# Kernel tuning notes

Measured on AMD Instinct MI355X. Metric: run time of the kernel, lower is better.

## Reference

```python
import jax, jax.numpy as jnp
import numpy as np

U = 100001          # user_count = user_num + 1
I = 50001           # item_count = item_num + 1
N = U + I           # total nodes
D = 64              # embedding dim
E = 3_200_000       # user-item interactions
NNZ = 2 * E         # symmetric directed edges
N_LAYERS = 3


def setup_inputs() -> dict:
    key = jax.random.key(0)
    k1, k2, k3, k4 = jax.random.split(key, 4)
    user_emb = jax.random.normal(k1, (U, D), dtype=jnp.float32) * 0.1
    item_emb = jax.random.normal(k2, (I, D), dtype=jnp.float32) * 0.1
    # random bipartite interactions, symmetrized like _get_a_adj_matrix
    u = jax.random.randint(k3, (E,), 0, U, dtype=jnp.int32)
    it = jax.random.randint(k4, (E,), 0, I, dtype=jnp.int32)
    rows = jnp.concatenate([u, it + U])            # [NNZ]
    cols = jnp.concatenate([it + U, u])            # [NNZ]
    # D^{-1/2} A D^{-1/2}: deg from row sums of A (values are 1s, duplicates sum)
    deg = jax.ops.segment_sum(jnp.ones((NNZ,), jnp.float32), rows, num_segments=N) + 1e-7
    dinv = deg ** -0.5
    vals = dinv[rows] * dinv[cols]                 # [NNZ]
    return {"user_emb": user_emb, "item_emb": item_emb,
            "rows": rows, "cols": cols, "vals": vals}


def _spmm(rows, cols, vals, x):
    # out[r] += vals * x[c]  (COO SpMM via gather + segment_sum)
    return jax.ops.segment_sum(vals[:, None] * x[cols], rows, num_segments=N)


def reference(user_emb, item_emb, rows, cols, vals):
    all_emb = jnp.concatenate([user_emb, item_emb], axis=0)   # [N, D]
    acc = all_emb                                             # running sum over layers (== mean * (L+1))
    h = all_emb
    for _ in range(N_LAYERS):
        h = _spmm(rows, cols, vals, h)
        acc = acc + h
    out = acc / (N_LAYERS + 1)                                # mean over stacked layers
    return out[:U], out[U:]
```

## Files before the change

### kernel.cpp

```cpp
#include <hip/hip_runtime.h>
#include <hip/hip_fp16.h>

#define U_CNT 100001
#define I_CNT 50001
#define N_CNT 150002
#define DIM 64
#define BROWS 128
#define NB2 ((N_CNT + BROWS - 1) / BROWS)
#define NB2R 1176
#define CH 6144
#define OUTCAP 10240

__device__ inline __half2 u2h(unsigned int u) { union { unsigned int u; __half2 h; } c; c.u = u; return c.h; }
__device__ inline unsigned int h2u(__half2 h) { union { unsigned int u; __half2 h; } c; c.h = h; return c.u; }

typedef float f4_t __attribute__((ext_vector_type(4)));
typedef unsigned int u4_t __attribute__((ext_vector_type(4)));

__device__ inline float4 ntload_f4(const float4* p) {
    f4_t v = __builtin_nontemporal_load((const f4_t*)p);
    return make_float4(v.x, v.y, v.z, v.w);
}
__device__ inline void ntstore_f4(float4* p, float4 v) {
    f4_t t; t.x = v.x; t.y = v.y; t.z = v.z; t.w = v.w;
    __builtin_nontemporal_store(t, (f4_t*)p);
}
__device__ inline void ntstore_u4(uint4* p, uint4 v) {
    u4_t t; t.x = v.x; t.y = v.y; t.z = v.z; t.w = v.w;
    __builtin_nontemporal_store(t, (u4_t*)p);
}

__global__ void bucket_hist(const int* __restrict__ rows, int* __restrict__ bhist,
                            int nnz) {
    __shared__ int lh[NB2];
    for (int i = threadIdx.x; i < NB2; i += blockDim.x) lh[i] = 0;
    __syncthreads();
    int stride = gridDim.x * blockDim.x;
    for (int i = blockIdx.x * blockDim.x + threadIdx.x; i < nnz; i += stride)
        atomicAdd(&lh[rows[i] >> 7], 1);
    __syncthreads();
    for (int i = threadIdx.x; i < NB2; i += blockDim.x) {
        int v = lh[i];
        if (v) atomicAdd(&bhist[i], v);
    }
}

__global__ void bucket_scan(const int* __restrict__ bhist,
                            int* __restrict__ bucket_ptr,
                            int* __restrict__ bcur) {
    __shared__ int aux[256];
    int t = threadIdx.x;
    int v[8];
    int s = 0;
    int b8 = t * 8;
    if (t < 147) {
        #pragma unroll
        for (int k = 0; k < 8; ++k) {
            int i = b8 + k;
            int d = (i < NB2) ? bhist[i] : 0;
            v[k] = s;
            s += d;
        }
    }
    aux[t] = s;
    __syncthreads();
    for (int off = 1; off < 256; off <<= 1) {
        int x = (t >= off) ? aux[t - off] : 0;
        __syncthreads();
        aux[t] += x;
        __syncthreads();
    }
    if (t < 147) {
        int gb = (t > 0) ? aux[t - 1] : 0;
        #pragma unroll
        for (int k = 0; k < 8; ++k) {
            int i = b8 + k;
            if (i < NB2) {
                int ex = gb + v[k];
                bucket_ptr[i] = ex;
                bcur[i] = ex;
            }
        }
    }
    if (t == 255) bucket_ptr[NB2] = aux[255];
}

__global__ void __launch_bounds__(256) partition_kernel(
    const int* __restrict__ rows, const int* __restrict__ cols,
    int* __restrict__ bcur, unsigned int* __restrict__ staging, int nnz)
{
    __shared__ int hist[NB2R];
    __shared__ int aux[256];
    __shared__ int gbase[NB2];
    __shared__ unsigned int recs[CH];
    __shared__ unsigned short guess[CH / 8];
    const int t = threadIdx.x;
    int base = blockIdx.x * CH;
    int lim = nnz - base; if (lim > CH) lim = CH;

    for (int i = t; i < NB2R; i += 256) hist[i] = 0;
    __syncthreads();
    for (int i = t; i < lim; i += 256)
        atomicAdd(&hist[rows[base + i] >> 7], 1);
    __syncthreads();
    {
        int s = 0;
        if (t < 147) {
            int b8 = t * 8;
            #pragma unroll
            for (int k = 0; k < 8; ++k) s += hist[b8 + k];
        }
        aux[t] = s;
    }
    __syncthreads();
    for (int off = 1; off < 256; off <<= 1) {
        int x = (t >= off) ? aux[t - off] : 0;
        __syncthreads();
        aux[t] += x;
        __syncthreads();
    }
    if (t < 147) {
        int run = (t > 0) ? aux[t - 1] : 0;
        int b8 = t * 8;
        #pragma unroll
        for (int k = 0; k < 8; ++k) {
            run += hist[b8 + k];
            hist[b8 + k] = run;
        }
    }
    __syncthreads();
    for (int i = t; i < NB2; i += 256) {
        int hi_ = hist[i];
        int lo_ = (i > 0) ? hist[i - 1] : 0;
        for (int m = (lo_ + 7) & ~7; m < hi_; m += 8)
            guess[m >> 3] = (unsigned short)i;
        int cnt = hi_ - lo_;
        if (cnt) gbase[i] = atomicAdd(&bcur[i], cnt);
    }
    __syncthreads();
    for (int i = t; i < lim; i += 256) {
        int r = rows[base + i];
        int c = cols[base + i];
        int p = atomicAdd(&hist[r >> 7], -1) - 1;
        recs[p] = ((unsigned int)c << 7) | (unsigned int)(r & (BROWS - 1));
    }
    __syncthreads();
    for (int p = t; p < lim; p += 256) {
        unsigned int rec = recs[p];
        int lo = guess[p >> 3];
        while (hist[lo + 1] <= p) ++lo;
        staging[gbase[lo] + (p - hist[lo])] = rec;
    }
}

__global__ void __launch_bounds__(256) binplace_kernel(
    const int* __restrict__ bucket_ptr,
    const unsigned int* __restrict__ staging,
    unsigned int* __restrict__ col_s,
    int* __restrict__ row_ptr,
    float* __restrict__ dinv) {
    __shared__ int hist[BROWS];
    __shared__ int cur[BROWS];
    __shared__ unsigned int outb[OUTCAP];
    int b = blockIdx.x;
    int base = b << 7;
    int beg = bucket_ptr[b];
    int end = bucket_ptr[b + 1];
    int total = end - beg;
    int t = threadIdx.x;
    if (t < BROWS) hist[t] = 0;
    __syncthreads();
    for (int j = beg + t; j < end; j += 256)
        atomicAdd(&hist[staging[j] & (BROWS - 1u)], 1);
    __syncthreads();
    int cnt = (t < BROWS) ? hist[t] : 0;
    for (int off = 1; off < BROWS; off <<= 1) {
        int v = (t < BROWS && t >= off) ? hist[t - off] : 0;
        __syncthreads();
        if (t < BROWS) hist[t] += v;
        __syncthreads();
    }
    if (t < BROWS) {
        int startl = hist[t] - cnt;
        cur[t] = startl;
        int r = base + t;
        if (r < N_CNT) {
            row_ptr[r] = beg + startl;
            dinv[r] = 1.0f / sqrtf((float)cnt + 1e-7f);
        }
    }
    if (b == NB2 - 1 && t == 0) row_ptr[N_CNT] = end;
    __syncthreads();
    if (total <= OUTCAP) {
        for (int j = beg + t; j < end; j += 256) {
            unsigned int rec = staging[j];
            int pos = atomicAdd(&cur[rec & (BROWS - 1u)], 1);
            outb[pos] = rec >> 7;
        }
        __syncthreads();
        for (int k = t; k < total; k += 256)
            col_s[beg + k] = outb[k];
    } else {
        for (int j = beg + t; j < end; j += 256) {
            unsigned int rec = staging[j];
            int pos = atomicAdd(&cur[rec & (BROWS - 1u)], 1);
            col_s[beg + pos] = rec >> 7;
        }
    }
}

__global__ void init_kernel(const float4* __restrict__ ue,
                            const float4* __restrict__ ie,
                            const float* __restrict__ dinv,
                            uint4* __restrict__ hs) {
    int i = blockIdx.x * blockDim.x + threadIdx.x;
    if (i >= N_CNT * 8) return;
    int node = i >> 3;
    int s = i & 7;
    float d = dinv[node];
    size_t fo = (size_t)node * 16 + s * 2;
    float4 v0, v1;
    if (node < U_CNT) { v0 = ntload_f4(&ue[fo]); v1 = ntload_f4(&ue[fo + 1]); }
    else { size_t io = fo - (size_t)U_CNT * 16; v0 = ntload_f4(&ie[io]); v1 = ntload_f4(&ie[io + 1]); }
    uint4 h;
    h.x = h2u(__floats2half2_rn(d * v0.x, d * v0.y));
    h.y = h2u(__floats2half2_rn(d * v0.z, d * v0.w));
    h.z = h2u(__floats2half2_rn(d * v1.x, d * v1.y));
    h.w = h2u(__floats2half2_rn(d * v1.z, d * v1.w));
    hs[(size_t)node * 8 + s] = h;
}

__device__ inline void acc8(float4& a0, float4& a1, uint4 u) {
    float2 f;
    f = __half22float2(u2h(u.x)); a0.x += f.x; a0.y += f.y;
    f = __half22float2(u2h(u.y)); a0.z += f.x; a0.w += f.y;
    f = __half22float2(u2h(u.z)); a1.x += f.x; a1.y += f.y;
    f = __half22float2(u2h(u.w)); a1.z += f.x; a1.w += f.y;
}

__global__ void spmm_gather(const int* __restrict__ row_ptr,
                            const unsigned int* __restrict__ col_s,
                            const float* __restrict__ dinv,
                            const uint4* __restrict__ x,
                            uint4* __restrict__ y,
                            const uint4* __restrict__ h1s,
                            const float4* __restrict__ ue,
                            const float4* __restrict__ ie,
                            float4* __restrict__ acc,
                            int r0, int r1, int last) {
    int r = r0 + blockIdx.x * 32 + (threadIdx.x >> 3);
    int s = threadIdx.x & 7;
    if (r >= r1) return;
    int beg = row_ptr[r];
    int end = row_ptr[r + 1];
    float4 a0 = {0.f, 0.f, 0.f, 0.f}, a1 = {0.f, 0.f, 0.f, 0.f};
    float4 b0 = {0.f, 0.f, 0.f, 0.f}, b1 = {0.f, 0.f, 0.f, 0.f};
    int j = beg;
    for (; j + 8 <= end; j += 8) {
        unsigned int c0 = col_s[j];
        unsigned int c1 = col_s[j + 1];
        unsigned int c2 = col_s[j + 2];
        unsigned int c3 = col_s[j + 3];
        unsigned int c4 = col_s[j + 4];
        unsigned int c5 = col_s[j + 5];
        unsigned int c6 = col_s[j + 6];
        unsigned int c7 = col_s[j + 7];
        uint4 u0 = x[(size_t)c0 * 8 + s];
        uint4 u1 = x[(size_t)c1 * 8 + s];
        uint4 u2 = x[(size_t)c2 * 8 + s];
        uint4 u3 = x[(size_t)c3 * 8 + s];
        uint4 u4 = x[(size_t)c4 * 8 + s];
        uint4 u5 = x[(size_t)c5 * 8 + s];
        uint4 u6 = x[(size_t)c6 * 8 + s];
        uint4 u7 = x[(size_t)c7 * 8 + s];
        acc8(a0, a1, u0);
        acc8(b0, b1, u1);
        acc8(a0, a1, u2);
        acc8(b0, b1, u3);
        acc8(a0, a1, u4);
        acc8(b0, b1, u5);
        acc8(a0, a1, u6);
        acc8(b0, b1, u7);
    }
    for (; j + 4 <= end; j += 4) {
        unsigned int c0 = col_s[j];
        unsigned int c1 = col_s[j + 1];
        unsigned int c2 = col_s[j + 2];
        unsigned int c3 = col_s[j + 3];
        uint4 u0 = x[(size_t)c0 * 8 + s];
        uint4 u1 = x[(size_t)c1 * 8 + s];
        uint4 u2 = x[(size_t)c2 * 8 + s];
        uint4 u3 = x[(size_t)c3 * 8 + s];
        acc8(a0, a1, u0);
        acc8(b0, b1, u1);
        acc8(a0, a1, u2);
        acc8(b0, b1, u3);
    }
    for (; j < end; ++j) {
        unsigned int c0 = col_s[j];
        uint4 u0 = x[(size_t)c0 * 8 + s];
        acc8(a0, a1, u0);
    }
    a0.x += b0.x; a0.y += b0.y; a0.z += b0.z; a0.w += b0.w;
    a1.x += b1.x; a1.y += b1.y; a1.z += b1.z; a1.w += b1.w;

    float d = dinv[r];
    if (!last) {
        float d2 = d * d;
        uint4 h;
        h.x = h2u(__floats2half2_rn(d2 * a0.x, d2 * a0.y));
        h.y = h2u(__floats2half2_rn(d2 * a0.z, d2 * a0.w));
        h.z = h2u(__floats2half2_rn(d2 * a1.x, d2 * a1.y));
        h.w = h2u(__floats2half2_rn(d2 * a1.z, d2 * a1.w));
        ntstore_u4(&y[(size_t)r * 8 + s], h);
        return;
    }

    float inv = 1.0f / d;
    uint4 u1 = h1s[(size_t)r * 8 + s];
    uint4 u2v = x[(size_t)r * 8 + s];
    float4 s0 = {0.f, 0.f, 0.f, 0.f}, s1 = {0.f, 0.f, 0.f, 0.f};
    acc8(s0, s1, u1);
    acc8(s0, s1, u2v);
    size_t fo = (size_t)r * 16 + s * 2;
    float4 e0a, e0b;
    if (r < U_CNT) { e0a = ntload_f4(&ue[fo]); e0b = ntload_f4(&ue[fo + 1]); }
    else { size_t io = fo - (size_t)U_CNT * 16; e0a = ntload_f4(&ie[io]); e0b = ntload_f4(&ie[io + 1]); }
    float4 o0, o1;
    o0.x = 0.25f * (e0a.x + inv * s0.x + d * a0.x);
    o0.y = 0.25f * (e0a.y + inv * s0.y + d * a0.y);
    o0.z = 0.25f * (e0a.z + inv * s0.z + d * a0.z);
    o0.w = 0.25f * (e0a.w + inv * s0.w + d * a0.w);
    o1.x = 0.25f * (e0b.x + inv * s1.x + d * a1.x);
    o1.y = 0.25f * (e0b.y + inv * s1.y + d * a1.y);
    o1.z = 0.25f * (e0b.z + inv * s1.z + d * a1.z);
    o1.w = 0.25f * (e0b.w + inv * s1.w + d * a1.w);
    ntstore_f4(&acc[fo], o0);
    ntstore_f4(&acc[fo + 1], o1);
}

extern "C" void kernel_launch(void* const* d_in, const int* in_sizes, int n_in,
                              void* d_out, int out_size, void* d_ws, size_t ws_size,
                              hipStream_t stream) {
    const float* ue   = (const float*)d_in[0];
    const float* ie   = (const float*)d_in[1];
    const int*   rows = (const int*)d_in[2];
    const int*   cols = (const int*)d_in[3];
    int nnz = in_sizes[2];

    float* acc = (float*)d_out;

    unsigned int* ws = (unsigned int*)d_ws;
    uint4* hs0 = (uint4*)ws;
    uint4* hs1 = hs0 + (size_t)N_CNT * 8;
    int*   row_ptr    = (int*)(hs1 + (size_t)N_CNT * 8);
    int*   bhist      = row_ptr + (N_CNT + 1);
    int*   bucket_ptr = bhist + NB2;
    int*   bcur       = bucket_ptr + (NB2 + 1);
    float* dinv       = (float*)(bcur + NB2);
    unsigned int* staging = (unsigned int*)(dinv + N_CNT);
    unsigned int* col_s   = staging + nnz;

    const int tpb = 256;

    hipMemsetAsync(bhist, 0, NB2 * sizeof(int), stream);
    bucket_hist<<<512, tpb, 0, stream>>>(rows, bhist, nnz);
    bucket_scan<<<1, 256, 0, stream>>>(bhist, bucket_ptr, bcur);
    partition_kernel<<<(nnz + CH - 1) / CH, tpb, 0, stream>>>(
        rows, cols, bcur, staging, nnz);
    binplace_kernel<<<NB2, tpb, 0, stream>>>(
        bucket_ptr, staging, col_s, row_ptr, dinv);

    init_kernel<<<(N_CNT * 8 + tpb - 1) / tpb, tpb, 0, stream>>>(
        (const float4*)ue, (const float4*)ie, dinv, hs0);

    uint4* cur_h = hs0;
    uint4* nxt_h = hs1;
    const int ublocks = (U_CNT + 31) / 32;
    const int iblocks = (N_CNT - U_CNT + 31) / 32;
    for (int l = 0; l < 3; ++l) {
        int last = (l == 2) ? 1 : 0;
        spmm_gather<<<ublocks, tpb, 0, stream>>>(
            row_ptr, col_s, dinv, cur_h, nxt_h, nxt_h,
            (const float4*)ue, (const float4*)ie, (float4*)acc, 0, U_CNT, last);
        spmm_gather<<<iblocks, tpb, 0, stream>>>(
            row_ptr, col_s, dinv, cur_h, nxt_h, nxt_h,
            (const float4*)ue, (const float4*)ie, (float4*)acc, U_CNT, N_CNT, last);
        uint4* tmp = cur_h; cur_h = nxt_h; nxt_h = tmp;
    }
}
```

Measured before the change: 565.8 us.

## Replace atomic bucket offsets with deterministic per-chunk count-scan partition

New measurement: 537.4 us. 5.0% less time.

```diff
diff --git a/kernel.cpp b/kernel.cpp
--- a/kernel.cpp
+++ b/kernel.cpp
@@ -30,24 +30,51 @@
     __builtin_nontemporal_store(t, (u4_t*)p);
 }
 
-__global__ void bucket_hist(const int* __restrict__ rows, int* __restrict__ bhist,
-                            int nnz) {
-    __shared__ int lh[NB2];
-    for (int i = threadIdx.x; i < NB2; i += blockDim.x) lh[i] = 0;
-    __syncthreads();
-    int stride = gridDim.x * blockDim.x;
-    for (int i = blockIdx.x * blockDim.x + threadIdx.x; i < nnz; i += stride)
-        atomicAdd(&lh[rows[i] >> 7], 1);
-    __syncthreads();
-    for (int i = threadIdx.x; i < NB2; i += blockDim.x) {
-        int v = lh[i];
-        if (v) atomicAdd(&bhist[i], v);
-    }
+
+__global__ void count_kernel(const int* __restrict__ rows, int* __restrict__ cnt,
+                             int nnz) {
+    __shared__ int lh[NB2R];
+    int t = threadIdx.x;
+    for (int i = t; i < NB2R; i += 256) lh[i] = 0;
+    __syncthreads();
+    int base = blockIdx.x * CH;
+    int lim = nnz - base; if (lim > CH) lim = CH;
+    for (int i = t; i < lim; i += 256)
+        atomicAdd(&lh[rows[base + i] >> 7], 1);
+    __syncthreads();
+    int* row = cnt + (size_t)blockIdx.x * NB2R;
+    for (int i = t; i < NB2R; i += 256) row[i] = lh[i];
+}
+
+__global__ void scan_chunks(const int* __restrict__ cnt, int* __restrict__ ex2,
+                            int* __restrict__ bhist, int nchunk) {
+    __shared__ int aux[256];
+    int b = blockIdx.x;
+    int t = threadIdx.x;
+    int G = (nchunk + 255) >> 8;
+    int c0 = t * G;
+    int c1 = c0 + G; if (c1 > nchunk) c1 = nchunk;
+    int s = 0;
+    for (int ch = c0; ch < c1; ++ch) s += cnt[(size_t)ch * NB2R + b];
+    aux[t] = s;
+    __syncthreads();
+    for (int off = 1; off < 256; off <<= 1) {
+        int x = (t >= off) ? aux[t - off] : 0;
+        __syncthreads();
+        aux[t] += x;
+        __syncthreads();
+    }
+    int run = (t > 0) ? aux[t - 1] : 0;
+    for (int ch = c0; ch < c1; ++ch) {
+        int v = cnt[(size_t)ch * NB2R + b];
+        ex2[(size_t)b * nchunk + ch] = run;
+        run += v;
+    }
+    if (t == 255) bhist[b] = aux[255];
 }
 
 __global__ void bucket_scan(const int* __restrict__ bhist,
-                            int* __restrict__ bucket_ptr,
-                            int* __restrict__ bcur) {
+                            int* __restrict__ bucket_ptr) {
     __shared__ int aux[256];
     int t = threadIdx.x;
     int v[8];
@@ -75,19 +102,17 @@
         #pragma unroll
         for (int k = 0; k < 8; ++k) {
             int i = b8 + k;
-            if (i < NB2) {
-                int ex = gb + v[k];
-                bucket_ptr[i] = ex;
-                bcur[i] = ex;
-            }
+            if (i < NB2) bucket_ptr[i] = gb + v[k];
         }
     }
     if (t == 255) bucket_ptr[NB2] = aux[255];
 }
 
-__global__ void __launch_bounds__(256) partition_kernel(
+__global__ void __launch_bounds__(256) fill_kernel(
     const int* __restrict__ rows, const int* __restrict__ cols,
-    int* __restrict__ bcur, unsigned int* __restrict__ staging, int nnz)
+    const int* __restrict__ cnt, const int* __restrict__ ex2,
+    const int* __restrict__ bucket_ptr,
+    unsigned int* __restrict__ staging, int nnz, int nchunk)
 {
     __shared__ int hist[NB2R];
     __shared__ int aux[256];
@@ -95,13 +120,14 @@
     __shared__ unsigned int recs[CH];
     __shared__ unsigned short guess[CH / 8];
     const int t = threadIdx.x;
-    int base = blockIdx.x * CH;
+    int chunk = blockIdx.x;
+    int base = chunk * CH;
     int lim = nnz - base; if (lim > CH) lim = CH;
 
-    for (int i = t; i < NB2R; i += 256) hist[i] = 0;
-    __syncthreads();
-    for (int i = t; i < lim; i += 256)
-        atomicAdd(&hist[rows[base + i] >> 7], 1);
+    const int* crow = cnt + (size_t)chunk * NB2R;
+    for (int i = t; i < NB2R; i += 256) hist[i] = crow[i];
+    for (int i = t; i < NB2; i += 256)
+        gbase[i] = bucket_ptr[i] + ex2[(size_t)i * nchunk + chunk];
     __syncthreads();
     {
         int s = 0;
@@ -134,8 +160,6 @@
         int lo_ = (i > 0) ? hist[i - 1] : 0;
         for (int m = (lo_ + 7) & ~7; m < hi_; m += 8)
             guess[m >> 3] = (unsigned short)i;
-        int cnt = hi_ - lo_;
-        if (cnt) gbase[i] = atomicAdd(&bcur[i], cnt);
     }
     __syncthreads();
     for (int i = t; i < lim; i += 256) {
@@ -347,6 +371,7 @@
     const int*   rows = (const int*)d_in[2];
     const int*   cols = (const int*)d_in[3];
     int nnz = in_sizes[2];
+    int nchunk = (nnz + CH - 1) / CH;
 
     float* acc = (float*)d_out;
 
@@ -356,18 +381,19 @@
     int*   row_ptr    = (int*)(hs1 + (size_t)N_CNT * 8);
     int*   bhist      = row_ptr + (N_CNT + 1);
     int*   bucket_ptr = bhist + NB2;
-    int*   bcur       = bucket_ptr + (NB2 + 1);
-    float* dinv       = (float*)(bcur + NB2);
+    float* dinv       = (float*)(bucket_ptr + NB2 + 1);
     unsigned int* staging = (unsigned int*)(dinv + N_CNT);
     unsigned int* col_s   = staging + nnz;
+    int* cnt = (int*)col_s;
+    int* ex2 = cnt + (size_t)nchunk * NB2R;
 
     const int tpb = 256;
 
-    hipMemsetAsync(bhist, 0, NB2 * sizeof(int), stream);
-    bucket_hist<<<512, tpb, 0, stream>>>(rows, bhist, nnz);
-    bucket_scan<<<1, 256, 0, stream>>>(bhist, bucket_ptr, bcur);
-    partition_kernel<<<(nnz + CH - 1) / CH, tpb, 0, stream>>>(
-        rows, cols, bcur, staging, nnz);
+    count_kernel<<<nchunk, tpb, 0, stream>>>(rows, cnt, nnz);
+    scan_chunks<<<NB2, tpb, 0, stream>>>(cnt, ex2, bhist, nchunk);
+    bucket_scan<<<1, tpb, 0, stream>>>(bhist, bucket_ptr);
+    fill_kernel<<<nchunk, tpb, 0, stream>>>(
+        rows, cols, cnt, ex2, bucket_ptr, staging, nnz, nchunk);
     binplace_kernel<<<NB2, tpb, 0, stream>>>(
         bucket_ptr, staging, col_s, row_ptr, dinv);
 
```
